# Optimization experiments

Hardware: AMD Instinct MI355X
Metric: run time of the kernel (lower is better)

The kernel has to match this reference:

```python
import jax, jax.numpy as jnp
import numpy as np

D_MODEL = 1024
N_HEADS = 16
D_K = D_MODEL // N_HEADS
LOCAL_WINDOW = 128
GLOBAL_TOKENS = 16


def sparse_mask(seq_len):
    i = jnp.arange(seq_len)[:, None]
    j = jnp.arange(seq_len)[None, :]
    local = jnp.abs(i - j) <= LOCAL_WINDOW
    glob = (i < GLOBAL_TOKENS) | (j < GLOBAL_TOKENS)
    causal = j <= i
    return ((local | glob) & causal)[None, None]  # [1,1,S,S]


def setup_inputs() -> dict:
    key = jax.random.key(0)
    ks = jax.random.split(key, 11)
    B, S = 2, 2048
    std = 1.0 / np.sqrt(D_MODEL)
    inp = {
        'query': jax.random.normal(ks[0], (B, S, D_MODEL), jnp.float32),
        'key': jax.random.normal(ks[1], (B, S, D_MODEL), jnp.float32),
        'value': jax.random.normal(ks[2], (B, S, D_MODEL), jnp.float32),
        'w_q': jax.random.normal(ks[3], (D_MODEL, D_MODEL), jnp.float32) * std,
        'b_q': jnp.zeros((D_MODEL,), jnp.float32),
        'w_k': jax.random.normal(ks[4], (D_MODEL, D_MODEL), jnp.float32) * std,
        'b_k': jnp.zeros((D_MODEL,), jnp.float32),
        'w_v': jax.random.normal(ks[5], (D_MODEL, D_MODEL), jnp.float32) * std,
        'b_v': jnp.zeros((D_MODEL,), jnp.float32),
        'w_o': jax.random.normal(ks[6], (D_MODEL, D_MODEL), jnp.float32) * std,
        'b_o': jnp.zeros((D_MODEL,), jnp.float32),
    }
    return inp


def reference(query, key, value, w_q, b_q, w_k, b_k, w_v, b_v, w_o, b_o):
    B, S, _ = query.shape
    # project and split heads -> [B,H,S,d_k]
    def proj(x, w, b):
        y = x @ w.T + b
        return y.reshape(B, S, N_HEADS, D_K).transpose(0, 2, 1, 3)
    q = proj(query, w_q, b_q)
    k = proj(key, w_k, b_k)
    v = proj(value, w_v, b_v)
    scores = jnp.einsum('bhqd,bhkd->bhqk', q, k) / np.sqrt(D_K).astype(np.float32)
    mask = sparse_mask(S)
    scores = jnp.where(mask, scores, -jnp.inf)
    attn = jax.nn.softmax(scores, axis=-1)
    out = jnp.einsum('bhqk,bhkd->bhqd', attn, v)
    out = out.transpose(0, 2, 1, 3).reshape(B, S, D_MODEL)
    return out @ w_o.T + b_o
```

## Files before the change

kernel.cpp:

```cpp
#include <hip/hip_runtime.h>

typedef unsigned short u16;
typedef u16 u16x8 __attribute__((ext_vector_type(8)));
typedef __bf16 bf16x8 __attribute__((ext_vector_type(8)));
typedef float f32x4 __attribute__((ext_vector_type(4)));

#define MFMA16 __builtin_amdgcn_mfma_f32_16x16x32_bf16

__device__ __forceinline__ u16 f2bf(float f) {
  unsigned u = __builtin_bit_cast(unsigned, f);
  u += 0x7FFFu + ((u >> 16) & 1u);
  return (u16)(u >> 16);
}

__device__ __forceinline__ int swz(int row, int bcol) {
  return row * 128 + (bcol ^ ((row & 7) << 4));
}

__device__ __forceinline__ void gl16(const u16* g, u16* l) {
  __builtin_amdgcn_global_load_lds(
      (const __attribute__((address_space(1))) unsigned int*)g,
      (__attribute__((address_space(3))) unsigned int*)l, 16, 0, 0);
}

__device__ __forceinline__ void BARR() {
  asm volatile("" ::: "memory");
  __builtin_amdgcn_s_barrier();
  asm volatile("" ::: "memory");
}
#define VMCNT(n) asm volatile("s_waitcnt vmcnt(" #n ")" ::: "memory")
#define LGKM0 asm volatile("s_waitcnt lgkmcnt(0)" ::: "memory")

__global__ __launch_bounds__(256)
void cast_all(const float* __restrict__ q, const float* __restrict__ k,
              const float* __restrict__ v, const float* __restrict__ wq,
              const float* __restrict__ wk, const float* __restrict__ wv,
              const float* __restrict__ wo, u16* __restrict__ ws) {
  const long i = ((long)blockIdx.x * 256 + threadIdx.x) * 8;
  const float* s;
  u16* d;
  if (i < 12582912) {
    const int seg = (int)(i >> 22);
    const float* xs = (seg == 0) ? q : (seg == 1) ? k : v;
    s = xs + (i & 4194303);
    d = ws + 4194304 + i;
  } else {
    const long j = i - 12582912;
    const int seg = (int)(j >> 20);
    const float* wsrc = (seg == 0) ? wq : (seg == 1) ? wk : (seg == 2) ? wv : wo;
    s = wsrc + (j & 1048575);
    d = ws + j;
  }
  float4 v0 = *(const float4*)s;
  float4 v1 = *(const float4*)(s + 4);
  u16x8 p = {f2bf(v0.x), f2bf(v0.y), f2bf(v0.z), f2bf(v0.w),
             f2bf(v1.x), f2bf(v1.y), f2bf(v1.z), f2bf(v1.w)};
  *(u16x8*)d = p;
}

#define ZSTGA(tt, j)                                                        \
  gl16(Ain + (m0 + (w << 5) + (j)*8 + (lane >> 3)) * 1024 + (tt)*64 +       \
           (((lane & 7) ^ (lane >> 3)) << 3),                               \
       (u16*)(sb + ((tt)&1) * 24576 + (w << 12) + ((j) << 10)))
#define ZSTGB(tt, j)                                                        \
  gl16(W + (n0 + (w << 4) + (j)*8 + (lane >> 3)) * 1024 + (tt)*64 +         \
           (((lane & 7) ^ (lane >> 3)) << 3),                               \
       (u16*)(sb + ((tt)&1) * 24576 + 16384 + (w << 11) + ((j) << 10)))
#define ZLDA()                                                              \
  _Pragma("unroll") for (int m = 0; m < 4; ++m) {                           \
    char* p = sb + bo + rowAb + m * 2048;                                   \
    af[0][m] = __builtin_bit_cast(bf16x8, *(const u16x8*)(p + colr0));      \
    af[1][m] = __builtin_bit_cast(bf16x8, *(const u16x8*)(p + colr1));      \
  }
#define ZLDB(n)                                                             \
  {                                                                         \
    char* p = sb + bo + rowBb + (n)*2048;                                   \
    bf[0][n] = __builtin_bit_cast(bf16x8, *(const u16x8*)(p + colr0));      \
    bf[1][n] = __builtin_bit_cast(bf16x8, *(const u16x8*)(p + colr1));      \
  }
#define ZFMA(n)                                                             \
  __builtin_amdgcn_s_setprio(1);                                            \
  _Pragma("unroll") for (int m = 0; m < 4; ++m) {                           \
    acc[m][n] = MFMA16(af[0][m], bf[0][n], acc[m][n], 0, 0, 0);             \
    acc[m][n] = MFMA16(af[1][m], bf[1][n], acc[m][n], 0, 0, 0);             \
  }                                                                         \
  __builtin_amdgcn_s_setprio(0);

__device__ __forceinline__ void core64(const u16* __restrict__ Ain,
                                       const u16* __restrict__ W, int m0,
                                       int n0, char* sb, f32x4 (&acc)[4][2]) {
  const int tid = threadIdx.x, lane = tid & 63, w = tid >> 6;
  const int wm = w >> 1, wn = w & 1;
  const int r = lane & 15, g = lane >> 4;
  bf16x8 af[2][4], bf[2][2];

  const int colr0 = (g * 16) ^ ((r & 7) << 4);
  const int colr1 = (64 + g * 16) ^ ((r & 7) << 4);
  const int rowAb = (wm * 64 + r) * 128;
  const int rowBb = 16384 + (wn * 32 + r) * 128;

#pragma unroll
  for (int j = 0; j < 4; ++j) ZSTGA(0, j);
#pragma unroll
  for (int j = 0; j < 2; ++j) ZSTGB(0, j);
#pragma unroll
  for (int j = 0; j < 4; ++j) ZSTGA(1, j);
  VMCNT(4);
  __builtin_amdgcn_s_barrier();
  asm volatile("" ::: "memory");

  for (int t = 0; t < 16; ++t) {
    const int bo = (t & 1) * 24576;
    if (t < 15) { ZSTGB(t + 1, 0); ZSTGB(t + 1, 1); }
    ZLDA();
    ZLDB(0);
    ZFMA(0);
    BARR();
    if (t < 14) { ZSTGA(t + 2, 0); ZSTGA(t + 2, 1); ZSTGA(t + 2, 2); ZSTGA(t + 2, 3); }
    ZLDB(1);
    ZFMA(1);
    if (t < 14) { VMCNT(4); } else if (t == 14) { VMCNT(0); }
    BARR();
  }
}

__global__ __launch_bounds__(256)
void qkv_gemm64(const u16* __restrict__ ws_in, const float* __restrict__ c0,
                const float* __restrict__ c1, const float* __restrict__ c2,
                u16* __restrict__ o0, u16* __restrict__ o1,
                u16* __restrict__ o2) {
  const int bid = blockIdx.x;
  const int s = (bid & 7) * 192 + (bid >> 3);
  const int z = s / 512;
  const int rem = s & 511;
  const int m0 = (rem >> 4) << 7;
  const int n0 = (rem & 15) << 6;

  const u16* __restrict__ Ain = ws_in + 4194304 + z * 4194304;
  const u16* __restrict__ W = ws_in + z * 1048576;
  const float* Bi = (z == 0) ? c0 : (z == 1) ? c1 : c2;
  u16* O = (z == 0) ? o0 : (z == 1) ? o1 : o2;

  const int tid = threadIdx.x, lane = tid & 63, w = tid >> 6;
  const int wm = w >> 1, wn = w & 1;
  const int r = lane & 15, g = lane >> 4;

  __shared__ u16 SH[24576];
  f32x4 acc[4][2] = {};
  core64(Ain, W, m0, n0, (char*)SH, acc);

#pragma unroll
  for (int n = 0; n < 2; ++n) {
    const int gn = n0 + wn * 32 + n * 16 + r;
    const int hh = gn >> 6, d = gn & 63;
    const float bv = Bi[gn];
#pragma unroll
    for (int m = 0; m < 4; ++m) {
#pragma unroll
      for (int q = 0; q < 4; ++q) {
        int gm = m0 + wm * 64 + m * 16 + g * 4 + q;
        int bb = gm >> 11, sIdx = gm & 2047;
        O[((bb * 16 + hh) * 2048 + sIdx) * 64 + d] = f2bf(acc[m][n][q] + bv);
      }
    }
  }
}

__global__ __launch_bounds__(256)
void out_gemm64(const u16* __restrict__ Ain, const u16* __restrict__ W,
                const float* __restrict__ Bi, float* __restrict__ C) {
  const int bid = blockIdx.x;
  const int s = (bid & 7) * 64 + (bid >> 3);
  const int m0 = (s >> 4) << 7;
  const int n0 = (s & 15) << 6;

  const int tid = threadIdx.x, lane = tid & 63, w = tid >> 6;
  const int wm = w >> 1, wn = w & 1;
  const int r = lane & 15, g = lane >> 4;

  __shared__ u16 SH[24576];
  f32x4 acc[4][2] = {};
  core64(Ain, W, m0, n0, (char*)SH, acc);

#pragma unroll
  for (int m = 0; m < 4; ++m) {
#pragma unroll
    for (int n = 0; n < 2; ++n) {
      int gn = n0 + wn * 32 + n * 16 + r;
      float bv = Bi[gn];
#pragma unroll
      for (int q = 0; q < 4; ++q) {
        int gm = m0 + wm * 64 + m * 16 + g * 4 + q;
        C[gm * 1024 + gn] = acc[m][n][q] + bv;
      }
    }
  }
}

__global__ __launch_bounds__(256)
void attn_kernel(const u16* __restrict__ Q, const u16* __restrict__ K,
                 const u16* __restrict__ V, u16* __restrict__ O) {
  const int qt = blockIdx.x, h = blockIdx.y, b = blockIdx.z;
  const int tid = threadIdx.x, lane = tid & 63, w = tid >> 6;
  const int r = lane & 15, g = lane >> 4;
  const int q0 = qt * 64;
  const int base = (b * 16 + h) * 131072;
  const u16* Qb = Q + base;

  __shared__ u16 Ks[2][4096];
  __shared__ u16 Vt[2][4096];
  __shared__ u16 Pl[4608];

  bf16x8 qf[2];
  {
    const u16* qp = Qb + (q0 + w * 16 + r) * 64 + g * 8;
    qf[0] = __builtin_bit_cast(bf16x8, *(const u16x8*)qp);
    qf[1] = __builtin_bit_cast(bf16x8, *(const u16x8*)(qp + 32));
  }

  f32x4 acc[4] = {};
  float m_run[4] = {-1e30f, -1e30f, -1e30f, -1e30f};
  float l_run[4] = {};

  const int nt = (qt <= 3) ? (qt + 1) : 4;
  const int srow = tid >> 3, sc = (tid & 7) * 8;
  const u16* Kg = K + base + srow * 64 + sc;
  const u16* Vg = V + base + srow * 64 + sc;

  u16x8 krA[2], vrA[2], krB[2], vrB[2];
  krA[0] = *(const u16x8*)(Kg);
  krA[1] = *(const u16x8*)(Kg + 2048);
  vrA[0] = *(const u16x8*)(Vg);
  vrA[1] = *(const u16x8*)(Vg + 2048);

#pragma unroll
  for (int tix = 0; tix < 4; ++tix) {
    if (tix < nt) {
      const int j0 = ((tix == 0) ? 0 : ((qt <= 3) ? tix : (qt - 3 + tix))) * 64;
      const int bo = (tix & 1) * 8192;
      if ((tix & 1) == 0) {
#pragma unroll
        for (int i = 0; i < 2; ++i) {
          int row = i * 32 + srow;
          *(u16x8*)((char*)Ks + bo + swz(row, sc * 2)) = krA[i];
#pragma unroll
          for (int qq = 0; qq < 8; ++qq) {
            int d = sc + qq;
            *(u16*)((char*)Vt + bo + d * 128 + ((2 * row) ^ ((d & 7) << 4))) =
                vrA[i][qq];
          }
        }
      } else {
#pragma unroll
        for (int i = 0; i < 2; ++i) {
          int row = i * 32 + srow;
          *(u16x8*)((char*)Ks + bo + swz(row, sc * 2)) = krB[i];
#pragma unroll
          for (int qq = 0; qq < 8; ++qq) {
            int d = sc + qq;
            *(u16*)((char*)Vt + bo + d * 128 + ((2 * row) ^ ((d & 7) << 4))) =
                vrB[i][qq];
          }
        }
      }
      if (tix + 1 < nt) {
        const int jn = (((qt <= 3) ? (tix + 1) : (qt - 2 + tix)) * 64) * 64;
        if ((tix & 1) == 0) {
          krB[0] = *(const u16x8*)(Kg + jn);
          krB[1] = *(const u16x8*)(Kg + jn + 2048);
          vrB[0] = *(const u16x8*)(Vg + jn);
          vrB[1] = *(const u16x8*)(Vg + jn + 2048);
        } else {
          krA[0] = *(const u16x8*)(Kg + jn);
          krA[1] = *(const u16x8*)(Kg + jn + 2048);
          vrA[0] = *(const u16x8*)(Vg + jn);
          vrA[1] = *(const u16x8*)(Vg + jn + 2048);
        }
      }
      LGKM0;
      BARR();

      f32x4 S[4] = {};
#pragma unroll
      for (int kk = 0; kk < 2; ++kk)
#pragma unroll
        for (int n = 0; n < 4; ++n) {
          bf16x8 kf = __builtin_bit_cast(
              bf16x8, *(const u16x8*)((char*)Ks + bo +
                                      swz(n * 16 + r, kk * 64 + g * 16)));
          S[n] = MFMA16(qf[kk], kf, S[n], 0, 0, 0);
        }

      float mloc[4] = {-1e30f, -1e30f, -1e30f, -1e30f};
#pragma unroll
      for (int n = 0; n < 4; ++n) {
        int j = j0 + n * 16 + r;
#pragma unroll
        for (int q = 0; q < 4; ++q) {
          int i = q0 + w * 16 + g * 4 + q;
          bool ok = (j <= i) && (((i - j) <= 128) || (j < 16));
          float s = ok ? S[n][q] * 0.125f : -1e30f;
          S[n][q] = s;
          mloc[q] = fmaxf(mloc[q], s);
        }
      }
#pragma unroll
      for (int q = 0; q < 4; ++q)
#pragma unroll
        for (int off = 1; off < 16; off <<= 1)
          mloc[q] = fmaxf(mloc[q], __shfl_xor(mloc[q], off));

      float alpha[4], rsum[4] = {};
#pragma unroll
      for (int q = 0; q < 4; ++q) {
        float mn = fmaxf(m_run[q], mloc[q]);
        alpha[q] = __expf(m_run[q] - mn);
        m_run[q] = mn;
      }
#pragma unroll
      for (int n = 0; n < 4; ++n)
#pragma unroll
        for (int q = 0; q < 4; ++q) {
          float p = __expf(S[n][q] - m_run[q]);
          S[n][q] = p;
          rsum[q] += p;
        }
#pragma unroll
      for (int q = 0; q < 4; ++q) {
#pragma unroll
        for (int off = 1; off < 16; off <<= 1)
          rsum[q] += __shfl_xor(rsum[q], off);
        l_run[q] = l_run[q] * alpha[q] + rsum[q];
      }
#pragma unroll
      for (int n = 0; n < 4; ++n) {
        acc[n][0] *= alpha[0];
        acc[n][1] *= alpha[1];
        acc[n][2] *= alpha[2];
        acc[n][3] *= alpha[3];
      }

#pragma unroll
      for (int n = 0; n < 4; ++n)
#pragma unroll
        for (int q = 0; q < 4; ++q)
          *((u16*)((char*)Pl + w * 2304 + (g * 4 + q) * 144) + (n * 16 + r)) =
              f2bf(S[n][q]);

#pragma unroll
      for (int kk = 0; kk < 2; ++kk) {
        bf16x8 pf = __builtin_bit_cast(
            bf16x8, *(const u16x8*)((char*)Pl + w * 2304 + r * 144 + kk * 64 +
                                    g * 16));
#pragma unroll
        for (int n = 0; n < 4; ++n) {
          bf16x8 vf = __builtin_bit_cast(
              bf16x8, *(const u16x8*)((char*)Vt + bo +
                                      swz(n * 16 + r, kk * 64 + g * 16)));
          acc[n] = MFMA16(pf, vf, acc[n], 0, 0, 0);
        }
      }
    }
  }

#pragma unroll
  for (int n = 0; n < 4; ++n)
#pragma unroll
    for (int q = 0; q < 4; ++q) {
      int s = q0 + w * 16 + g * 4 + q;
      int d = n * 16 + r;
      O[(b * 2048 + s) * 1024 + h * 64 + d] = f2bf(acc[n][q] / l_run[q]);
    }
}

extern "C" void kernel_launch(void* const* d_in, const int* in_sizes, int n_in,
                              void* d_out, int out_size, void* d_ws,
                              size_t ws_size, hipStream_t stream) {
  const float* b_q = (const float*)d_in[4];
  const float* b_k = (const float*)d_in[6];
  const float* b_v = (const float*)d_in[8];
  const float* b_o = (const float*)d_in[10];

  u16* ws = (u16*)d_ws;
  u16* Qw = ws + 16777216;
  u16* Kw = ws + 20971520;
  u16* Vw = ws + 25165824;
  u16* Aw = ws + 4194304;

  cast_all<<<dim3(8192), dim3(256), 0, stream>>>(
      (const float*)d_in[0], (const float*)d_in[1], (const float*)d_in[2],
      (const float*)d_in[3], (const float*)d_in[5], (const float*)d_in[7],
      (const float*)d_in[9], ws);
  qkv_gemm64<<<dim3(1536), dim3(256), 0, stream>>>(ws, b_q, b_k, b_v, Qw, Kw,
                                                   Vw);
  attn_kernel<<<dim3(32, 16, 2), dim3(256), 0, stream>>>(Qw, Kw, Vw, Aw);
  out_gemm64<<<dim3(512), dim3(256), 0, stream>>>(Aw, ws + 3145728, b_o,
                                                  (float*)d_out);
}
```

Measured before the change: 89.06 us.

## Fuse fp32-to-bf16 activation cast into QKV projection GEMM

```diff
diff --git a/kernel.cpp b/kernel.cpp
--- a/kernel.cpp
+++ b/kernel.cpp
@@ -13,6 +13,11 @@
   return (u16)(u >> 16);
 }
 
+__device__ __forceinline__ bf16x8 cvt8(float4 a, float4 b) {
+  return (bf16x8){(__bf16)a.x, (__bf16)a.y, (__bf16)a.z, (__bf16)a.w,
+                  (__bf16)b.x, (__bf16)b.y, (__bf16)b.z, (__bf16)b.w};
+}
+
 __device__ __forceinline__ int swz(int row, int bcol) {
   return row * 128 + (bcol ^ ((row & 7) << 4));
 }
@@ -32,30 +37,134 @@
 #define LGKM0 asm volatile("s_waitcnt lgkmcnt(0)" ::: "memory")
 
 __global__ __launch_bounds__(256)
-void cast_all(const float* __restrict__ q, const float* __restrict__ k,
-              const float* __restrict__ v, const float* __restrict__ wq,
-              const float* __restrict__ wk, const float* __restrict__ wv,
-              const float* __restrict__ wo, u16* __restrict__ ws) {
-  const long i = ((long)blockIdx.x * 256 + threadIdx.x) * 8;
-  const float* s;
-  u16* d;
-  if (i < 12582912) {
-    const int seg = (int)(i >> 22);
-    const float* xs = (seg == 0) ? q : (seg == 1) ? k : v;
-    s = xs + (i & 4194303);
-    d = ws + 4194304 + i;
-  } else {
-    const long j = i - 12582912;
-    const int seg = (int)(j >> 20);
-    const float* wsrc = (seg == 0) ? wq : (seg == 1) ? wk : (seg == 2) ? wv : wo;
-    s = wsrc + (j & 1048575);
-    d = ws + j;
-  }
+void cast_w(const float* __restrict__ wq, const float* __restrict__ wk,
+            const float* __restrict__ wv, const float* __restrict__ wo,
+            u16* __restrict__ ws) {
+  const int i = (blockIdx.x * 256 + threadIdx.x) * 8;
+  const int seg = i >> 20;
+  const float* s =
+      ((seg == 0) ? wq : (seg == 1) ? wk : (seg == 2) ? wv : wo) + (i & 1048575);
   float4 v0 = *(const float4*)s;
   float4 v1 = *(const float4*)(s + 4);
   u16x8 p = {f2bf(v0.x), f2bf(v0.y), f2bf(v0.z), f2bf(v0.w),
              f2bf(v1.x), f2bf(v1.y), f2bf(v1.z), f2bf(v1.w)};
-  *(u16x8*)d = p;
+  *(u16x8*)(ws + i) = p;
+}
+
+#define FSTGA(tt, j)                                                        \
+  gl16((const u16*)(((j)&1 ? srcO : srcE) + (j)*4096 + (tt)*64),            \
+       (u16*)(sb + (((tt)&1) << 15) + (((w << 3) + (j)) << 10)))
+#define FSTGB(tt, j)                                                        \
+  gl16(W + (n0 + (w << 4) + (j)*8 + (lane >> 3)) * 1024 + (tt)*64 +         \
+           (((lane & 7) ^ (lane >> 3)) << 3),                               \
+       (u16*)(sb + 65536 + (((tt)&1) << 13) + (w << 11) + ((j) << 10)))
+#define FLDA()                                                              \
+  _Pragma("unroll") for (int m = 0; m < 4; ++m) {                           \
+    const char* p = sb + boA + rowAf + m * 4096;                            \
+    float4 x0 = *(const float4*)(p + ca0);                                  \
+    float4 x1 = *(const float4*)(p + ca1);                                  \
+    float4 x2 = *(const float4*)(p + ca2);                                  \
+    float4 x3 = *(const float4*)(p + ca3);                                  \
+    af[0][m] = cvt8(x0, x1);                                                \
+    af[1][m] = cvt8(x2, x3);                                                \
+  }
+#define FLDB(n)                                                             \
+  {                                                                         \
+    const char* p = sb + 65536 + boB + rowBf + (n)*2048;                    \
+    bf[0][n] = __builtin_bit_cast(bf16x8, *(const u16x8*)(p + colr0));      \
+    bf[1][n] = __builtin_bit_cast(bf16x8, *(const u16x8*)(p + colr1));      \
+  }
+#define FFMA(n)                                                             \
+  __builtin_amdgcn_s_setprio(1);                                            \
+  _Pragma("unroll") for (int m = 0; m < 4; ++m) {                           \
+    acc[m][n] = MFMA16(af[0][m], bf[0][n], acc[m][n], 0, 0, 0);             \
+    acc[m][n] = MFMA16(af[1][m], bf[1][n], acc[m][n], 0, 0, 0);             \
+  }                                                                         \
+  __builtin_amdgcn_s_setprio(0);
+
+__global__ __launch_bounds__(256)
+void qkv_f32(const float* __restrict__ Xq, const float* __restrict__ Xk,
+             const float* __restrict__ Xv, const u16* __restrict__ Wall,
+             const float* __restrict__ bq, const float* __restrict__ bk,
+             const float* __restrict__ bv, u16* __restrict__ Qw,
+             u16* __restrict__ Kw, u16* __restrict__ Vw) {
+  const int bid = blockIdx.x;
+  const int s = (bid & 7) * 192 + (bid >> 3);
+  const int z = s / 512;
+  const int rem = s & 511;
+  const int m0 = (rem >> 4) << 7;
+  const int n0 = (rem & 15) << 6;
+
+  const float* __restrict__ X = (z == 0) ? Xq : (z == 1) ? Xk : Xv;
+  const u16* __restrict__ W = Wall + z * 1048576;
+  const float* Bi = (z == 0) ? bq : (z == 1) ? bk : bv;
+  u16* O = (z == 0) ? Qw : (z == 1) ? Kw : Vw;
+
+  const int tid = threadIdx.x, lane = tid & 63, w = tid >> 6;
+  const int wm = w >> 1, wn = w & 1;
+  const int r = lane & 15, g = lane >> 4;
+
+  __shared__ u16 SH[40960];
+  char* sb = (char*)SH;
+
+  f32x4 acc[4][2] = {};
+  bf16x8 af[2][4], bf[2][2];
+
+  const float* srcE = X + (m0 + (w << 5) + g) * 1024 + ((r ^ g) << 2);
+  const float* srcO = X + (m0 + (w << 5) + g) * 1024 + (((r ^ g) << 2) ^ 16);
+
+  const int rowAf = (wm * 64 + r) * 256;
+  const int ca0 = ((2 * g) ^ (r & 7)) << 4;
+  const int ca1 = ((2 * g + 1) ^ (r & 7)) << 4;
+  const int ca2 = ((8 + 2 * g) ^ (r & 7)) << 4;
+  const int ca3 = ((9 + 2 * g) ^ (r & 7)) << 4;
+  const int rowBf = (wn * 32 + r) * 128;
+  const int colr0 = (g * 16) ^ ((r & 7) << 4);
+  const int colr1 = (64 + g * 16) ^ ((r & 7) << 4);
+
+#pragma unroll
+  for (int j = 0; j < 8; ++j) FSTGA(0, j);
+  FSTGB(0, 0);
+  FSTGB(0, 1);
+#pragma unroll
+  for (int j = 0; j < 8; ++j) FSTGA(1, j);
+  VMCNT(8);
+  __builtin_amdgcn_s_barrier();
+  asm volatile("" ::: "memory");
+
+  for (int t = 0; t < 16; ++t) {
+    const int boA = (t & 1) << 15;
+    const int boB = (t & 1) << 13;
+    if (t < 15) { FSTGB(t + 1, 0); FSTGB(t + 1, 1); }
+    FLDA();
+    FLDB(0);
+    FFMA(0);
+    BARR();
+    if (t < 14) {
+#pragma unroll
+      for (int j = 0; j < 8; ++j) FSTGA(t + 2, j);
+    }
+    FLDB(1);
+    FFMA(1);
+    if (t < 14) { VMCNT(8); } else if (t == 14) { VMCNT(0); }
+    BARR();
+  }
+
+#pragma unroll
+  for (int n = 0; n < 2; ++n) {
+    const int gn = n0 + wn * 32 + n * 16 + r;
+    const int hh = gn >> 6, d = gn & 63;
+    const float bv = Bi[gn];
+#pragma unroll
+    for (int m = 0; m < 4; ++m) {
+#pragma unroll
+      for (int q = 0; q < 4; ++q) {
+        int gm = m0 + wm * 64 + m * 16 + g * 4 + q;
+        int bb = gm >> 11, sIdx = gm & 2047;
+        O[((bb * 16 + hh) * 2048 + sIdx) * 64 + d] = f2bf(acc[m][n][q] + bv);
+      }
+    }
+  }
 }
 
 #define ZSTGA(tt, j)                                                        \
@@ -125,48 +234,6 @@
 }
 
 __global__ __launch_bounds__(256)
-void qkv_gemm64(const u16* __restrict__ ws_in, const float* __restrict__ c0,
-                const float* __restrict__ c1, const float* __restrict__ c2,
-                u16* __restrict__ o0, u16* __restrict__ o1,
-                u16* __restrict__ o2) {
-  const int bid = blockIdx.x;
-  const int s = (bid & 7) * 192 + (bid >> 3);
-  const int z = s / 512;
-  const int rem = s & 511;
-  const int m0 = (rem >> 4) << 7;
-  const int n0 = (rem & 15) << 6;
-
-  const u16* __restrict__ Ain = ws_in + 4194304 + z * 4194304;
-  const u16* __restrict__ W = ws_in + z * 1048576;
-  const float* Bi = (z == 0) ? c0 : (z == 1) ? c1 : c2;
-  u16* O = (z == 0) ? o0 : (z == 1) ? o1 : o2;
-
-  const int tid = threadIdx.x, lane = tid & 63, w = tid >> 6;
-  const int wm = w >> 1, wn = w & 1;
-  const int r = lane & 15, g = lane >> 4;
-
-  __shared__ u16 SH[24576];
-  f32x4 acc[4][2] = {};
-  core64(Ain, W, m0, n0, (char*)SH, acc);
-
-#pragma unroll
-  for (int n = 0; n < 2; ++n) {
-    const int gn = n0 + wn * 32 + n * 16 + r;
-    const int hh = gn >> 6, d = gn & 63;
-    const float bv = Bi[gn];
-#pragma unroll
-    for (int m = 0; m < 4; ++m) {
-#pragma unroll
-      for (int q = 0; q < 4; ++q) {
-        int gm = m0 + wm * 64 + m * 16 + g * 4 + q;
-        int bb = gm >> 11, sIdx = gm & 2047;
-        O[((bb * 16 + hh) * 2048 + sIdx) * 64 + d] = f2bf(acc[m][n][q] + bv);
-      }
-    }
-  }
-}
-
-__global__ __launch_bounds__(256)
 void out_gemm64(const u16* __restrict__ Ain, const u16* __restrict__ W,
                 const float* __restrict__ Bi, float* __restrict__ C) {
   const int bid = blockIdx.x;
@@ -376,23 +443,25 @@
 extern "C" void kernel_launch(void* const* d_in, const int* in_sizes, int n_in,
                               void* d_out, int out_size, void* d_ws,
                               size_t ws_size, hipStream_t stream) {
+  const float* query = (const float*)d_in[0];
+  const float* key = (const float*)d_in[1];
+  const float* value = (const float*)d_in[2];
   const float* b_q = (const float*)d_in[4];
   const float* b_k = (const float*)d_in[6];
   const float* b_v = (const float*)d_in[8];
   const float* b_o = (const float*)d_in[10];
 
   u16* ws = (u16*)d_ws;
-  u16* Qw = ws + 16777216;
-  u16* Kw = ws + 20971520;
-  u16* Vw = ws + 25165824;
-  u16* Aw = ws + 4194304;
-
-  cast_all<<<dim3(8192), dim3(256), 0, stream>>>(
-      (const float*)d_in[0], (const float*)d_in[1], (const float*)d_in[2],
+  u16* Qw = ws + 4194304;
+  u16* Kw = ws + 8388608;
+  u16* Vw = ws + 12582912;
+  u16* Aw = ws + 16777216;
+
+  cast_w<<<dim3(2048), dim3(256), 0, stream>>>(
       (const float*)d_in[3], (const float*)d_in[5], (const float*)d_in[7],
       (const float*)d_in[9], ws);
-  qkv_gemm64<<<dim3(1536), dim3(256), 0, stream>>>(ws, b_q, b_k, b_v, Qw, Kw,
-                                                   Vw);
+  qkv_f32<<<dim3(1536), dim3(256), 0, stream>>>(query, key, value, ws, b_q,
+                                                b_k, b_v, Qw, Kw, Vw);
   attn_kernel<<<dim3(32, 16, 2), dim3(256), 0, stream>>>(Qw, Kw, Vw, Aw);
   out_gemm64<<<dim3(512), dim3(256), 0, stream>>>(Aw, ws + 3145728, b_o,
                                                   (float*)d_out);
```

Result: slower. 110.1 us (+23.7%).

## Fuse cast, QKV GEMM, attention and output GEMM into one cooperative persistent kernel

Applied to the files above, without the earlier changes.

```diff
diff --git a/kernel.cpp b/kernel.cpp
--- a/kernel.cpp
+++ b/kernel.cpp
@@ -1,4 +1,7 @@
 #include <hip/hip_runtime.h>
+#include <hip/hip_cooperative_groups.h>
+
+namespace cg = cooperative_groups;
 
 typedef unsigned short u16;
 typedef u16 u16x8 __attribute__((ext_vector_type(8)));
@@ -30,33 +33,6 @@
 }
 #define VMCNT(n) asm volatile("s_waitcnt vmcnt(" #n ")" ::: "memory")
 #define LGKM0 asm volatile("s_waitcnt lgkmcnt(0)" ::: "memory")
-
-__global__ __launch_bounds__(256)
-void cast_all(const float* __restrict__ q, const float* __restrict__ k,
-              const float* __restrict__ v, const float* __restrict__ wq,
-              const float* __restrict__ wk, const float* __restrict__ wv,
-              const float* __restrict__ wo, u16* __restrict__ ws) {
-  const long i = ((long)blockIdx.x * 256 + threadIdx.x) * 8;
-  const float* s;
-  u16* d;
-  if (i < 12582912) {
-    const int seg = (int)(i >> 22);
-    const float* xs = (seg == 0) ? q : (seg == 1) ? k : v;
-    s = xs + (i & 4194303);
-    d = ws + 4194304 + i;
-  } else {
-    const long j = i - 12582912;
-    const int seg = (int)(j >> 20);
-    const float* wsrc = (seg == 0) ? wq : (seg == 1) ? wk : (seg == 2) ? wv : wo;
-    s = wsrc + (j & 1048575);
-    d = ws + j;
-  }
-  float4 v0 = *(const float4*)s;
-  float4 v1 = *(const float4*)(s + 4);
-  u16x8 p = {f2bf(v0.x), f2bf(v0.y), f2bf(v0.z), f2bf(v0.w),
-             f2bf(v1.x), f2bf(v1.y), f2bf(v1.z), f2bf(v1.w)};
-  *(u16x8*)d = p;
-}
 
 #define ZSTGA(tt, j)                                                        \
   gl16(Ain + (m0 + (w << 5) + (j)*8 + (lane >> 3)) * 1024 + (tt)*64 +       \
@@ -124,20 +100,17 @@
   }
 }
 
-__global__ __launch_bounds__(256)
-void qkv_gemm64(const u16* __restrict__ ws_in, const float* __restrict__ c0,
-                const float* __restrict__ c1, const float* __restrict__ c2,
-                u16* __restrict__ o0, u16* __restrict__ o1,
-                u16* __restrict__ o2) {
-  const int bid = blockIdx.x;
-  const int s = (bid & 7) * 192 + (bid >> 3);
+__device__ void qkv_tile(int vt, const u16* __restrict__ ws, const float* c0,
+                         const float* c1, const float* c2, u16* o0, u16* o1,
+                         u16* o2, char* sb) {
+  const int s = (vt & 7) * 192 + (vt >> 3);
   const int z = s / 512;
   const int rem = s & 511;
   const int m0 = (rem >> 4) << 7;
   const int n0 = (rem & 15) << 6;
 
-  const u16* __restrict__ Ain = ws_in + 4194304 + z * 4194304;
-  const u16* __restrict__ W = ws_in + z * 1048576;
+  const u16* __restrict__ Ain = ws + 4194304 + z * 4194304;
+  const u16* __restrict__ W = ws + z * 1048576;
   const float* Bi = (z == 0) ? c0 : (z == 1) ? c1 : c2;
   u16* O = (z == 0) ? o0 : (z == 1) ? o1 : o2;
 
@@ -145,9 +118,8 @@
   const int wm = w >> 1, wn = w & 1;
   const int r = lane & 15, g = lane >> 4;
 
-  __shared__ u16 SH[24576];
   f32x4 acc[4][2] = {};
-  core64(Ain, W, m0, n0, (char*)SH, acc);
+  core64(Ain, W, m0, n0, sb, acc);
 
 #pragma unroll
   for (int n = 0; n < 2; ++n) {
@@ -166,11 +138,10 @@
   }
 }
 
-__global__ __launch_bounds__(256)
-void out_gemm64(const u16* __restrict__ Ain, const u16* __restrict__ W,
-                const float* __restrict__ Bi, float* __restrict__ C) {
-  const int bid = blockIdx.x;
-  const int s = (bid & 7) * 64 + (bid >> 3);
+__device__ void out_tile(int vo, const u16* __restrict__ Ain,
+                         const u16* __restrict__ W, const float* Bi, float* C,
+                         char* sb) {
+  const int s = (vo & 7) * 64 + (vo >> 3);
   const int m0 = (s >> 4) << 7;
   const int n0 = (s & 15) << 6;
 
@@ -178,9 +149,8 @@
   const int wm = w >> 1, wn = w & 1;
   const int r = lane & 15, g = lane >> 4;
 
-  __shared__ u16 SH[24576];
   f32x4 acc[4][2] = {};
-  core64(Ain, W, m0, n0, (char*)SH, acc);
+  core64(Ain, W, m0, n0, sb, acc);
 
 #pragma unroll
   for (int m = 0; m < 4; ++m) {
@@ -197,19 +167,19 @@
   }
 }
 
-__global__ __launch_bounds__(256)
-void attn_kernel(const u16* __restrict__ Q, const u16* __restrict__ K,
-                 const u16* __restrict__ V, u16* __restrict__ O) {
-  const int qt = blockIdx.x, h = blockIdx.y, b = blockIdx.z;
+__device__ void attn_vb(int vb, const u16* __restrict__ Q,
+                        const u16* __restrict__ K, const u16* __restrict__ V,
+                        u16* __restrict__ O, char* shp) {
+  const int qt = vb & 31, h = (vb >> 5) & 15, b = vb >> 9;
   const int tid = threadIdx.x, lane = tid & 63, w = tid >> 6;
   const int r = lane & 15, g = lane >> 4;
   const int q0 = qt * 64;
   const int base = (b * 16 + h) * 131072;
   const u16* Qb = Q + base;
 
-  __shared__ u16 Ks[2][4096];
-  __shared__ u16 Vt[2][4096];
-  __shared__ u16 Pl[4608];
+  u16* Ks = (u16*)shp;
+  u16* Vt = (u16*)(shp + 16384);
+  u16* Pl = (u16*)(shp + 32768);
 
   bf16x8 qf[2];
   {
@@ -371,29 +341,87 @@
       int d = n * 16 + r;
       O[(b * 2048 + s) * 1024 + h * 64 + d] = f2bf(acc[n][q] / l_run[q]);
     }
+  BARR();
+}
+
+__global__ __launch_bounds__(256)
+void fused_all(const float* __restrict__ q, const float* __restrict__ k,
+               const float* __restrict__ v, const float* __restrict__ wq,
+               const float* __restrict__ wk, const float* __restrict__ wv,
+               const float* __restrict__ wo, const float* __restrict__ bq,
+               const float* __restrict__ bk, const float* __restrict__ bv,
+               const float* __restrict__ bo_, u16* __restrict__ ws,
+               float* __restrict__ outp) {
+  __shared__ char SH[49152];
+  cg::grid_group grid = cg::this_grid();
+  const int bid = blockIdx.x, tid = threadIdx.x;
+
+  for (long i = ((long)bid * 256 + tid) * 8; i < 16777216;
+       i += (long)gridDim.x * 2048) {
+    const float* s;
+    u16* d;
+    if (i < 12582912) {
+      const int seg = (int)(i >> 22);
+      const float* xs = (seg == 0) ? q : (seg == 1) ? k : v;
+      s = xs + (i & 4194303);
+      d = ws + 4194304 + i;
+    } else {
+      const long j = i - 12582912;
+      const int seg = (int)(j >> 20);
+      const float* wsrc =
+          (seg == 0) ? wq : (seg == 1) ? wk : (seg == 2) ? wv : wo;
+      s = wsrc + (j & 1048575);
+      d = ws + j;
+    }
+    float4 v0 = *(const float4*)s;
+    float4 v1 = *(const float4*)(s + 4);
+    u16x8 p = {f2bf(v0.x), f2bf(v0.y), f2bf(v0.z), f2bf(v0.w),
+               f2bf(v1.x), f2bf(v1.y), f2bf(v1.z), f2bf(v1.w)};
+    *(u16x8*)d = p;
+  }
+  grid.sync();
+
+  u16* Qw = ws + 16777216;
+  u16* Kw = ws + 20971520;
+  u16* Vw = ws + 25165824;
+  for (int vt = bid; vt < 1536; vt += gridDim.x)
+    qkv_tile(vt, ws, bq, bk, bv, Qw, Kw, Vw, SH);
+  grid.sync();
+
+  u16* Aw = ws + 4194304;
+  for (int vb = bid; vb < 1024; vb += gridDim.x)
+    attn_vb(vb, Qw, Kw, Vw, Aw, SH);
+  grid.sync();
+
+  for (int vo = bid; vo < 512; vo += gridDim.x)
+    out_tile(vo, Aw, ws + 3145728, bo_, outp, SH);
 }
 
 extern "C" void kernel_launch(void* const* d_in, const int* in_sizes, int n_in,
                               void* d_out, int out_size, void* d_ws,
                               size_t ws_size, hipStream_t stream) {
-  const float* b_q = (const float*)d_in[4];
-  const float* b_k = (const float*)d_in[6];
-  const float* b_v = (const float*)d_in[8];
-  const float* b_o = (const float*)d_in[10];
-
+  const float* q = (const float*)d_in[0];
+  const float* k = (const float*)d_in[1];
+  const float* v = (const float*)d_in[2];
+  const float* wq = (const float*)d_in[3];
+  const float* bq = (const float*)d_in[4];
+  const float* wk = (const float*)d_in[5];
+  const float* bk = (const float*)d_in[6];
+  const float* wv = (const float*)d_in[7];
+  const float* bv = (const float*)d_in[8];
+  const float* wo = (const float*)d_in[9];
+  const float* bo_ = (const float*)d_in[10];
   u16* ws = (u16*)d_ws;
-  u16* Qw = ws + 16777216;
-  u16* Kw = ws + 20971520;
-  u16* Vw = ws + 25165824;
-  u16* Aw = ws + 4194304;
-
-  cast_all<<<dim3(8192), dim3(256), 0, stream>>>(
-      (const float*)d_in[0], (const float*)d_in[1], (const float*)d_in[2],
-      (const float*)d_in[3], (const float*)d_in[5], (const float*)d_in[7],
-      (const float*)d_in[9], ws);
-  qkv_gemm64<<<dim3(1536), dim3(256), 0, stream>>>(ws, b_q, b_k, b_v, Qw, Kw,
-                                                   Vw);
-  attn_kernel<<<dim3(32, 16, 2), dim3(256), 0, stream>>>(Qw, Kw, Vw, Aw);
-  out_gemm64<<<dim3(512), dim3(256), 0, stream>>>(Aw, ws + 3145728, b_o,
-                                                  (float*)d_out);
-}
+  float* outp = (float*)d_out;
+
+  int maxB = 0;
+  hipOccupancyMaxActiveBlocksPerMultiprocessor(&maxB, fused_all, 256, 0);
+  if (maxB < 1) maxB = 1;
+  if (maxB > 3) maxB = 3;
+  const int grid = 256 * maxB;
+
+  void* args[] = {&q,  &k,  &v,  &wq, &wk, &wv,  &wo,
+                  &bq, &bk, &bv, &bo_, &ws, &outp};
+  hipLaunchCooperativeKernel(fused_all, dim3(grid), dim3(256), args, 0,
+                             stream);
+}
```

New measurement: 211.1 us. 137% more time.
